# Kernel tuning notes

Measured on AMD Instinct MI355X. Metric: run time of the kernel, lower is better.

## Reference

```python
import jax, jax.numpy as jnp
import numpy as np

NUM_CLASSES = 80
SCORE_THRESHOLD = 0.05
MAX_DETECTIONS = 300


def setup_inputs() -> dict:
    key = jax.random.key(0)
    k1, k2, k3 = jax.random.split(key, 3)
    B, Q, C = 256, 1000, NUM_CLASSES
    pred_logits = jax.random.normal(k1, (B, Q, C), dtype=jnp.float32)
    # cxcywh boxes in normalized coords (cx,cy in ~(0,1), w,h small positive)
    pred_boxes = jax.random.uniform(k2, (B, Q, 4), dtype=jnp.float32, minval=0.05, maxval=0.6)
    # (height, width) per image, realistic pixel sizes
    target_sizes = jnp.floor(jax.random.uniform(k3, (B, 2), dtype=jnp.float32, minval=224.0, maxval=1024.0))
    return {"pred_logits": pred_logits, "pred_boxes": pred_boxes, "target_sizes": target_sizes}


def reference(pred_logits, pred_boxes, target_sizes):
    # focal-loss path: per-class sigmoid, then max over classes
    prob = jax.nn.sigmoid(pred_logits)                # [B, Q, C]
    scores = jnp.max(prob, axis=-1)                   # [B, Q]
    labels = jnp.argmax(prob, axis=-1)                # [B, Q]

    # cxcywh -> xyxy
    cx, cy, w, h = jnp.split(pred_boxes, 4, axis=-1)  # each [B, Q, 1]
    boxes = jnp.concatenate(
        [cx - 0.5 * w, cy - 0.5 * h, cx + 0.5 * w, cy + 0.5 * h], axis=-1
    )                                                 # [B, Q, 4]

    img_h = target_sizes[:, 0]
    img_w = target_sizes[:, 1]
    scale_fct = jnp.stack([img_w, img_h, img_w, img_h], axis=1)  # [B, 4]
    boxes = boxes * scale_fct[:, None, :]

    # score threshold via sentinel mask, then fixed-size per-image top-k
    masked_scores = jnp.where(scores > SCORE_THRESHOLD, scores, -1.0)
    top_scores, top_idx = jax.lax.top_k(masked_scores, MAX_DETECTIONS)  # [B, K]
    valid = top_scores > SCORE_THRESHOLD                               # [B, K]

    out_scores = jnp.where(valid, top_scores, 0.0)
    out_labels = jnp.where(valid, jnp.take_along_axis(labels, top_idx, axis=1), -1)
    out_boxes = jnp.where(
        valid[..., None],
        jnp.take_along_axis(boxes, top_idx[..., None], axis=1),
        0.0,
    )
    return out_scores, out_labels, out_boxes
```

## Files before the change

### kernel.cpp

```cpp
#include <hip/hip_runtime.h>
#include <math.h>

#define BATCH   256
#define NQ      1000
#define NC      80
#define NDET    300
#define SCORE_TH 0.05f

typedef unsigned long long u64;

#define A_THREADS 256

__global__ __launch_bounds__(A_THREADS) void rtdetr_phase1(
    const float* __restrict__ logits,
    u64* __restrict__ keys64)
{
    const int t    = threadIdx.x;
    const int lane = t & 63;
    const int wid  = t >> 6;
    const int b    = blockIdx.x >> 4;
    const int q    = (blockIdx.x & 15) * 64 + wid * 16 + (lane >> 2);
    const int r    = lane & 3;

    if (q >= NQ) return;

    const float4* g = (const float4*)(logits + (size_t)b * NQ * NC) + (size_t)q * 20;

    float bv = -1e30f;
    int   bc = 0;
    #pragma unroll
    for (int i = 0; i < 5; ++i) {
        float4 v = g[4 * i + r];
        int c = 16 * i + 4 * r;
        if (v.x > bv) { bv = v.x; bc = c + 0; }
        if (v.y > bv) { bv = v.y; bc = c + 1; }
        if (v.z > bv) { bv = v.z; bc = c + 2; }
        if (v.w > bv) { bv = v.w; bc = c + 3; }
    }
    #pragma unroll
    for (int d = 1; d <= 2; d <<= 1) {
        float ov = __shfl_xor(bv, d);
        int   oc = __shfl_xor(bc, d);
        if (ov > bv || (ov == bv && oc < bc)) { bv = ov; bc = oc; }
    }
    if (r == 0) {
        float sc = 1.0f / (1.0f + expf(-bv));
        unsigned int key = (sc > SCORE_TH) ? __float_as_uint(sc) : 0u;
        keys64[(size_t)b * NQ + q] =
            ((u64)key << 32) | ((unsigned int)(1023 - q) << 10) | (unsigned int)bc;
    }
}

#define B_THREADS 1024

__global__ __launch_bounds__(B_THREADS) void rtdetr_phase2(
    const u64* __restrict__ keys64,
    const float* __restrict__ boxes,
    const float* __restrict__ sizes,
    float* __restrict__ out)
{
    __shared__ u64 s_k[B_THREADS];

    const int b = blockIdx.x;
    const int t = threadIdx.x;

    u64 v = (t < NQ) ? keys64[(size_t)b * NQ + t] : 0ull;

    for (int k = 2; k <= B_THREADS; k <<= 1) {
        for (int j = k >> 1; j > 0; j >>= 1) {
            u64 o;
            if (j >= 64) {
                s_k[t] = v;
                __syncthreads();
                o = s_k[t ^ j];
                __syncthreads();
            } else {
                o = __shfl_xor(v, j);
            }
            const bool takeMax = (((t & j) == 0) == ((t & k) == 0));
            if (takeMax ? (o > v) : (o < v)) v = o;
        }
    }

    if (t < NDET) {
        unsigned int key = (unsigned int)(v >> 32);

        float* out_scores = out;
        float* out_labels = out + (size_t)BATCH * NDET;
        float* out_boxes  = out + (size_t)2 * BATCH * NDET;
        const int o = b * NDET + t;

        if (key != 0u) {
            int lab = (int)(v & 0x3FFull);
            int idx = 1023 - (int)((v >> 10) & 0x3FFull);
            out_scores[o] = __uint_as_float(key);
            out_labels[o] = (float)lab;
            float4 bx = ((const float4*)boxes)[b * NQ + idx];
            const float img_h = sizes[2 * b + 0];
            const float img_w = sizes[2 * b + 1];
            float4 ob;
            ob.x = (bx.x - 0.5f * bx.z) * img_w;
            ob.y = (bx.y - 0.5f * bx.w) * img_h;
            ob.z = (bx.x + 0.5f * bx.z) * img_w;
            ob.w = (bx.y + 0.5f * bx.w) * img_h;
            ((float4*)out_boxes)[o] = ob;
        } else {
            out_scores[o] = 0.0f;
            out_labels[o] = -1.0f;
            ((float4*)out_boxes)[o] = make_float4(0.0f, 0.0f, 0.0f, 0.0f);
        }
    }
}

extern "C" void kernel_launch(void* const* d_in, const int* in_sizes, int n_in,
                              void* d_out, int out_size, void* d_ws, size_t ws_size,
                              hipStream_t stream) {
    const float* logits = (const float*)d_in[0];
    const float* boxes  = (const float*)d_in[1];
    const float* sizes  = (const float*)d_in[2];
    float* out = (float*)d_out;

    u64* keys64 = (u64*)d_ws;

    rtdetr_phase1<<<BATCH * 16, A_THREADS, 0, stream>>>(logits, keys64);
    rtdetr_phase2<<<BATCH, B_THREADS, 0, stream>>>(keys64, boxes, sizes, out);
}
```

Measured before the change: 133.7 us.

## Fuse class-max and per-image bitonic top-k into one kernel

Merges the two kernels into a single per-image kernel of 1024 threads. Each block computes the per-query max-class keys straight into shared memory, then runs the bitonic sort on them. Boxes are also staged in LDS before the gather. This removes the workspace round trip and one launch, but the whole logits read now runs on only 256 blocks. That means fewer waves in flight to hide memory latency than with the 4096-block first phase.

```diff
diff --git a/kernel.cpp b/kernel.cpp
--- a/kernel.cpp
+++ b/kernel.cpp
@@ -5,75 +5,69 @@
 #define NQ      1000
 #define NC      80
 #define NDET    300
+#define THREADS 1024
 #define SCORE_TH 0.05f
 
 typedef unsigned long long u64;
 
-#define A_THREADS 256
-
-__global__ __launch_bounds__(A_THREADS) void rtdetr_phase1(
+__global__ __launch_bounds__(THREADS) void rtdetr_fused(
     const float* __restrict__ logits,
-    u64* __restrict__ keys64)
-{
-    const int t    = threadIdx.x;
-    const int lane = t & 63;
-    const int wid  = t >> 6;
-    const int b    = blockIdx.x >> 4;
-    const int q    = (blockIdx.x & 15) * 64 + wid * 16 + (lane >> 2);
-    const int r    = lane & 3;
-
-    if (q >= NQ) return;
-
-    const float4* g = (const float4*)(logits + (size_t)b * NQ * NC) + (size_t)q * 20;
-
-    float bv = -1e30f;
-    int   bc = 0;
-    #pragma unroll
-    for (int i = 0; i < 5; ++i) {
-        float4 v = g[4 * i + r];
-        int c = 16 * i + 4 * r;
-        if (v.x > bv) { bv = v.x; bc = c + 0; }
-        if (v.y > bv) { bv = v.y; bc = c + 1; }
-        if (v.z > bv) { bv = v.z; bc = c + 2; }
-        if (v.w > bv) { bv = v.w; bc = c + 3; }
-    }
-    #pragma unroll
-    for (int d = 1; d <= 2; d <<= 1) {
-        float ov = __shfl_xor(bv, d);
-        int   oc = __shfl_xor(bc, d);
-        if (ov > bv || (ov == bv && oc < bc)) { bv = ov; bc = oc; }
-    }
-    if (r == 0) {
-        float sc = 1.0f / (1.0f + expf(-bv));
-        unsigned int key = (sc > SCORE_TH) ? __float_as_uint(sc) : 0u;
-        keys64[(size_t)b * NQ + q] =
-            ((u64)key << 32) | ((unsigned int)(1023 - q) << 10) | (unsigned int)bc;
-    }
-}
-
-#define B_THREADS 1024
-
-__global__ __launch_bounds__(B_THREADS) void rtdetr_phase2(
-    const u64* __restrict__ keys64,
     const float* __restrict__ boxes,
     const float* __restrict__ sizes,
     float* __restrict__ out)
 {
-    __shared__ u64 s_k[B_THREADS];
+    __shared__ u64    s_k[THREADS];
+    __shared__ float4 s_box[NQ];
 
     const int b = blockIdx.x;
     const int t = threadIdx.x;
 
-    u64 v = (t < NQ) ? keys64[(size_t)b * NQ + t] : 0ull;
+    if (t < NQ) s_box[t] = ((const float4*)boxes)[b * NQ + t];
+    if (t >= NQ) s_k[t] = 0ull;
 
-    for (int k = 2; k <= B_THREADS; k <<= 1) {
+    const int r = t & 3;
+    const float4* gbase = (const float4*)(logits + (size_t)b * NQ * NC);
+    #pragma unroll
+    for (int p = 0; p < 4; ++p) {
+        const int q = p * 256 + (t >> 2);
+        if (q < NQ) {
+            const float4* g = gbase + (size_t)q * 20;
+            float bv = -1e30f;
+            int   bc = 0;
+            #pragma unroll
+            for (int i = 0; i < 5; ++i) {
+                float4 v = g[4 * i + r];
+                int c = 16 * i + 4 * r;
+                if (v.x > bv) { bv = v.x; bc = c + 0; }
+                if (v.y > bv) { bv = v.y; bc = c + 1; }
+                if (v.z > bv) { bv = v.z; bc = c + 2; }
+                if (v.w > bv) { bv = v.w; bc = c + 3; }
+            }
+            #pragma unroll
+            for (int d = 1; d <= 2; d <<= 1) {
+                float ov = __shfl_xor(bv, d);
+                int   oc = __shfl_xor(bc, d);
+                if (ov > bv || (ov == bv && oc < bc)) { bv = ov; bc = oc; }
+            }
+            if (r == 0) {
+                float sc = 1.0f / (1.0f + expf(-bv));
+                unsigned int key = (sc > SCORE_TH) ? __float_as_uint(sc) : 0u;
+                s_k[q] = ((u64)key << 32) |
+                         ((unsigned int)(1023 - q) << 10) | (unsigned int)bc;
+            }
+        }
+    }
+    __syncthreads();
+
+    u64 v = s_k[t];
+    for (int k = 2; k <= THREADS; k <<= 1) {
         for (int j = k >> 1; j > 0; j >>= 1) {
             u64 o;
             if (j >= 64) {
+                __syncthreads();
                 s_k[t] = v;
                 __syncthreads();
                 o = s_k[t ^ j];
-                __syncthreads();
             } else {
                 o = __shfl_xor(v, j);
             }
@@ -95,7 +89,7 @@
             int idx = 1023 - (int)((v >> 10) & 0x3FFull);
             out_scores[o] = __uint_as_float(key);
             out_labels[o] = (float)lab;
-            float4 bx = ((const float4*)boxes)[b * NQ + idx];
+            float4 bx = s_box[idx];
             const float img_h = sizes[2 * b + 0];
             const float img_w = sizes[2 * b + 1];
             float4 ob;
@@ -120,8 +114,5 @@
     const float* sizes  = (const float*)d_in[2];
     float* out = (float*)d_out;
 
-    u64* keys64 = (u64*)d_ws;
-
-    rtdetr_phase1<<<BATCH * 16, A_THREADS, 0, stream>>>(logits, keys64);
-    rtdetr_phase2<<<BATCH, B_THREADS, 0, stream>>>(keys64, boxes, sizes, out);
+    rtdetr_fused<<<BATCH, THREADS, 0, stream>>>(logits, boxes, sizes, out);
 }
```

Result: no change. 131.6 us (-1.6%).
